# Performance work log

Hardware: AMD Instinct MI355X
Metric: run time of the kernel (lower is better)

The kernel has to match this reference:

```python
import jax, jax.numpy as jnp
import numpy as np

DIM = 2048          # SDR dimension
CTX = 512           # top-down context (grid code) dimension
B = 8192            # batch of independent samples
N_PV = DIM // 4     # 512 PV interneurons
N_SV = DIM // 8     # 256 SOM/VIP interneurons
ALPHA_POS = 1.0 / 10.0   # dt / tau_pos
ALPHA_NEG = 1.0 / 10.0   # dt / tau_neg


def setup_inputs() -> dict:
    key = jax.random.key(0)
    ks = jax.random.split(key, 14)
    sc = 1.0 / np.sqrt(DIM)
    sc_sv = 1.0 / np.sqrt(N_SV)
    xav = np.sqrt(6.0 / (CTX + DIM))  # xavier uniform bound for predictor
    u = lambda k, shp, s: jax.random.uniform(k, shp, dtype=jnp.float32) * s
    return {
        "x_batch": jax.random.uniform(ks[0], (B, DIM), dtype=jnp.float32),
        "context_batch": jax.random.normal(ks[1], (B, CTX), dtype=jnp.float32),
        "r_pos_batch": jax.random.uniform(ks[2], (B, DIM), dtype=jnp.float32),
        "r_neg_batch": jax.random.uniform(ks[3], (B, DIM), dtype=jnp.float32),
        "W_pred": jax.random.uniform(ks[4], (DIM, CTX), jnp.float32, -xav, xav),
        "b_pred": jnp.zeros((DIM,), jnp.float32),
        "W_pv1_ff": u(ks[5], (N_PV, DIM), sc),
        "W_pv2_td": u(ks[6], (N_PV, DIM), sc),
        "W_vip_td": u(ks[7], (N_SV, DIM), sc),
        "W_som_in": u(ks[8], (N_SV, DIM), sc),
        "W_vip_som": u(ks[9], (N_SV, N_SV), sc_sv),
        "W_inh_pe_pos": u(ks[10], (DIM, N_PV), sc),
        "W_inh_pe_neg": u(ks[11], (DIM, N_PV), sc),
        "W_som_dend": u(ks[12], (DIM, N_SV), sc),
    }


def reference(x_batch, context_batch, r_pos_batch, r_neg_batch,
              W_pred, b_pred, W_pv1_ff, W_pv2_td, W_vip_td, W_som_in,
              W_vip_som, W_inh_pe_pos, W_inh_pe_neg, W_som_dend):
    relu = jax.nn.relu
    # top-down prediction: (B, CTX) @ (CTX, DIM) -> (B, DIM)
    predicted = context_batch @ W_pred.T + b_pred
    # interneuron circuit (Nemati 2025)
    r_pv1 = relu(x_batch @ W_pv1_ff.T)                               # (B, N_PV)
    r_pv2 = relu(predicted @ W_pv2_td.T)                             # (B, N_PV)
    r_vip = relu(predicted @ W_vip_td.T)                             # (B, N_SV)
    r_som = relu(relu(x_batch @ W_som_in.T) - r_vip @ W_vip_som.T)   # (B, N_SV)
    # signed prediction errors with somatic/dendritic inhibition
    pe_pos = relu(x_batch - predicted - r_pv2 @ W_inh_pe_pos.T)
    pe_neg = relu(predicted - x_batch - r_pv1 @ W_inh_pe_neg.T - r_som @ W_som_dend.T)
    # low-pass temporal filter of PE states
    new_r_pos = (1.0 - ALPHA_POS) * r_pos_batch + ALPHA_POS * pe_pos
    new_r_neg = (1.0 - ALPHA_NEG) * r_neg_batch + ALPHA_NEG * pe_neg
    return (new_r_pos, new_r_neg)
```

## Files before the change

### kernel.cpp

```cpp
#include <hip/hip_runtime.h>
#include <hip/hip_bf16.h>
#include <stdint.h>
#include <stddef.h>

#define DIMV 2048
#define CTXV 512
#define BV   8192
#define NPV  512
#define NSV  256

typedef __attribute__((ext_vector_type(8))) __bf16 bf16x8;
typedef __attribute__((ext_vector_type(4))) float f32x4;

enum { EPI_BIAS = 0, EPI_RELU = 1, EPI_SUBR = 2, EPI_FILT = 3 };

__device__ __forceinline__ void gload_lds16(const void* g, void* l) {
    __builtin_amdgcn_global_load_lds(
        (const __attribute__((address_space(1))) unsigned int*)g,
        (__attribute__((address_space(3))) unsigned int*)l,
        16, 0, 0);
}

struct CvtArgs {
    const float* src[11];
    __bf16*      dst[11];
};

__global__ __launch_bounds__(256) void cvt_all(CvtArgs a) {
    constexpr int NSEG = 11;
    constexpr unsigned cum[NSEG + 1] = {
        0u, 2097152u, 2621440u, 2752512u, 2883584u, 3014656u,
        3080192u, 3145728u, 3153920u, 3284992u, 3416064u, 3481600u};
    const unsigned total = cum[NSEG];
    for (unsigned c = blockIdx.x * blockDim.x + threadIdx.x; c < total;
         c += gridDim.x * blockDim.x) {
        const float* sp = a.src[0];
        __bf16*      dp = a.dst[0];
        unsigned     base = 0;
#pragma unroll
        for (int t = 1; t < NSEG; ++t) {
            const bool g = (c >= cum[t]);
            sp   = g ? a.src[t] : sp;
            dp   = g ? a.dst[t] : dp;
            base = g ? cum[t] : base;
        }
        const unsigned off = (c - base) * 8u;
        f32x4 v0 = *(const f32x4*)(sp + off);
        f32x4 v1 = *(const f32x4*)(sp + off + 4);
        bf16x8 o;
#pragma unroll
        for (int e = 0; e < 4; ++e) { o[e] = (__bf16)v0[e]; o[e + 4] = (__bf16)v1[e]; }
        *(bf16x8*)(dp + off) = o;
    }
}

template <int EPI>
__global__ __launch_bounds__(256)
void pe_gemm(const __bf16* __restrict__ A, int ldA,
             const __bf16* __restrict__ A2, int ldA2, int ksA,
             const __bf16* __restrict__ W1, int ldW1,
             const __bf16* __restrict__ W1k2, int ldW1k2, int ksW,
             const __bf16* __restrict__ W2, int ldW2,
             int NB1, int N1cols, int N2cols, int K, int nbx,
             const float* __restrict__ bias,
             const __bf16* __restrict__ subp,
             const __bf16* __restrict__ predb, const float* __restrict__ xf,
             float sgn, const float* __restrict__ rold,
             void* __restrict__ out1, void* __restrict__ out2)
{
    __shared__ __align__(16) __bf16 ldsA[128 * 32];
    __shared__ __align__(16) __bf16 ldsB[128 * 32];
    char* ldsAb = (char*)ldsA;
    char* ldsBb = (char*)ldsB;

    const int nwg = gridDim.x;
    const int bid = blockIdx.x;
    const int wg  = (bid & 7) * (nwg >> 3) + (bid >> 3);
    const int bx  = wg % nbx;
    const int by  = wg / nbx;
    const int m0  = bx * 128;
    const int n0  = by * 128;

    const bool reg2   = (W2 != nullptr) && (n0 >= NB1);
    const __bf16* Wa  = reg2 ? W2 : W1;
    const __bf16* Wb  = W1k2;
    const int wlda    = reg2 ? ldW2 : ldW1;
    const int wldb    = ldW1k2;
    const int kswcur  = reg2 ? K : ksW;
    const int nrow0   = reg2 ? (n0 - NB1) : n0;

    const int tid  = threadIdx.x;
    const int wave = tid >> 6;
    const int lane = tid & 63;
    const int lhi  = lane >> 4;
    const int llo  = lane & 15;
    const int wr   = wave >> 1;
    const int wc   = wave & 1;

    const f32x4 fzero = {0.f, 0.f, 0.f, 0.f};
    f32x4 acc[4][4];
#pragma unroll
    for (int i = 0; i < 4; ++i)
#pragma unroll
        for (int j = 0; j < 4; ++j) acc[i][j] = fzero;

    const int rins = lane >> 2;
    const int ch   = lane & 3;

    for (int k0 = 0; k0 < K; k0 += 32) {
        __syncthreads();
#pragma unroll
        for (int half = 0; half < 2; ++half) {
            const int rt = wave * 32 + half * 16 + rins;
            const int kc = ch ^ ((rt >> 1) & 3);
            const int kg = k0 + kc * 8;
            {
                const __bf16* src = (kg < ksA)
                    ? A  + (size_t)(m0 + rt) * ldA  + kg
                    : A2 + (size_t)(m0 + rt) * ldA2 + (kg - ksA);
                gload_lds16(src, ldsAb + wave * 2048 + half * 1024);
            }
            {
                const __bf16* src = (kg < kswcur)
                    ? Wa + (size_t)(nrow0 + rt) * wlda + kg
                    : Wb + (size_t)(nrow0 + rt) * wldb + (kg - kswcur);
                gload_lds16(src, ldsBb + wave * 2048 + half * 1024);
            }
        }
        __syncthreads();

        bf16x8 af[4], bfr[4];
#pragma unroll
        for (int i = 0; i < 4; ++i) {
            const int r  = wr * 64 + i * 16 + llo;
            const int pc = lhi ^ ((r >> 1) & 3);
            af[i] = *(const bf16x8*)(ldsAb + r * 64 + pc * 16);
        }
#pragma unroll
        for (int j = 0; j < 4; ++j) {
            const int r  = wc * 64 + j * 16 + llo;
            const int pc = lhi ^ ((r >> 1) & 3);
            bfr[j] = *(const bf16x8*)(ldsBb + r * 64 + pc * 16);
        }
#pragma unroll
        for (int i = 0; i < 4; ++i)
#pragma unroll
            for (int j = 0; j < 4; ++j)
                acc[i][j] = __builtin_amdgcn_mfma_f32_16x16x32_bf16(af[i], bfr[j], acc[i][j], 0, 0, 0);
    }

#pragma unroll
    for (int i = 0; i < 4; ++i) {
#pragma unroll
        for (int j = 0; j < 4; ++j) {
            const int colg = n0 + wc * 64 + j * 16 + llo;
#pragma unroll
            for (int r = 0; r < 4; ++r) {
                const int rowg = m0 + wr * 64 + i * 16 + lhi * 4 + r;
                float v = acc[i][j][r];
                if constexpr (EPI == EPI_BIAS) {
                    v += bias[colg];
                    ((__bf16*)out1)[(size_t)rowg * N1cols + colg] = (__bf16)v;
                } else if constexpr (EPI == EPI_RELU) {
                    v = fmaxf(v, 0.f);
                    if (colg < NB1)
                        ((__bf16*)out1)[(size_t)rowg * N1cols + colg] = (__bf16)v;
                    else
                        ((__bf16*)out2)[(size_t)rowg * N2cols + (colg - NB1)] = (__bf16)v;
                } else if constexpr (EPI == EPI_SUBR) {
                    const size_t idx = (size_t)rowg * N1cols + colg;
                    v = fmaxf((float)subp[idx] - v, 0.f);
                    ((__bf16*)out1)[idx] = (__bf16)v;
                } else {
                    const size_t idx = (size_t)rowg * 2048 + colg;
                    const float d = sgn * (xf[idx] - (float)predb[idx]) - v;
                    ((float*)out1)[idx] = 0.9f * rold[idx] + 0.1f * fmaxf(d, 0.f);
                }
            }
        }
    }
}

extern "C" void kernel_launch(void* const* d_in, const int* in_sizes, int n_in,
                              void* d_out, int out_size, void* d_ws, size_t ws_size,
                              hipStream_t stream) {
    (void)in_sizes; (void)n_in; (void)out_size; (void)ws_size;

    const float* x       = (const float*)d_in[0];
    const float* ctx     = (const float*)d_in[1];
    const float* r_pos   = (const float*)d_in[2];
    const float* r_neg   = (const float*)d_in[3];
    const float* Wpred   = (const float*)d_in[4];
    const float* bpred   = (const float*)d_in[5];
    const float* Wpv1    = (const float*)d_in[6];
    const float* Wpv2    = (const float*)d_in[7];
    const float* Wvip    = (const float*)d_in[8];
    const float* Wsomin  = (const float*)d_in[9];
    const float* Wvipsom = (const float*)d_in[10];
    const float* Wpepos  = (const float*)d_in[11];
    const float* Wpeneg  = (const float*)d_in[12];
    const float* Wsomd   = (const float*)d_in[13];

    char* ws = (char*)d_ws;
    __bf16* x_bf      = (__bf16*)ws; ws += (size_t)BV * DIMV * 2;
    __bf16* ctx_bf    = (__bf16*)ws; ws += (size_t)BV * CTXV * 2;
    __bf16* pred_bf   = (__bf16*)ws; ws += (size_t)BV * DIMV * 2;
    __bf16* rpv1_bf   = (__bf16*)ws; ws += (size_t)BV * NPV * 2;
    __bf16* rpv2_bf   = (__bf16*)ws; ws += (size_t)BV * NPV * 2;
    __bf16* rvip_bf   = (__bf16*)ws; ws += (size_t)BV * NSV * 2;
    __bf16* ssom_bf   = (__bf16*)ws; ws += (size_t)BV * NSV * 2;
    __bf16* rsom_bf   = (__bf16*)ws; ws += (size_t)BV * NSV * 2;
    __bf16* Wpred_bf  = (__bf16*)ws; ws += (size_t)DIMV * CTXV * 2;
    __bf16* Wpv1_bf   = (__bf16*)ws; ws += (size_t)NPV * DIMV * 2;
    __bf16* Wpv2_bf   = (__bf16*)ws; ws += (size_t)NPV * DIMV * 2;
    __bf16* Wvip_bf   = (__bf16*)ws; ws += (size_t)NSV * DIMV * 2;
    __bf16* Wsomin_bf = (__bf16*)ws; ws += (size_t)NSV * DIMV * 2;
    __bf16* Wvipsom_bf= (__bf16*)ws; ws += (size_t)NSV * NSV * 2;
    __bf16* Wpepos_bf = (__bf16*)ws; ws += (size_t)DIMV * NPV * 2;
    __bf16* Wpeneg_bf = (__bf16*)ws; ws += (size_t)DIMV * NPV * 2;
    __bf16* Wsomd_bf  = (__bf16*)ws; ws += (size_t)DIMV * NSV * 2;

    float* out_pos = (float*)d_out;
    float* out_neg = out_pos + (size_t)BV * DIMV;

    CvtArgs ca;
    ca.src[0] = x;       ca.dst[0] = x_bf;
    ca.src[1] = ctx;     ca.dst[1] = ctx_bf;
    ca.src[2] = Wpred;   ca.dst[2] = Wpred_bf;
    ca.src[3] = Wpv1;    ca.dst[3] = Wpv1_bf;
    ca.src[4] = Wpv2;    ca.dst[4] = Wpv2_bf;
    ca.src[5] = Wvip;    ca.dst[5] = Wvip_bf;
    ca.src[6] = Wsomin;  ca.dst[6] = Wsomin_bf;
    ca.src[7] = Wvipsom; ca.dst[7] = Wvipsom_bf;
    ca.src[8] = Wpepos;  ca.dst[8] = Wpepos_bf;
    ca.src[9] = Wpeneg;  ca.dst[9] = Wpeneg_bf;
    ca.src[10] = Wsomd;  ca.dst[10] = Wsomd_bf;
    cvt_all<<<dim3(2048), dim3(256), 0, stream>>>(ca);

    dim3 blk(256);

    pe_gemm<EPI_BIAS><<<dim3(1024), blk, 0, stream>>>(
        ctx_bf, CTXV, nullptr, 0, CTXV,
        Wpred_bf, CTXV, nullptr, 0, CTXV, nullptr, 0,
        DIMV, DIMV, 0, CTXV, 64,
        bpred, nullptr, nullptr, nullptr, 0.f, nullptr, pred_bf, nullptr);

    pe_gemm<EPI_RELU><<<dim3(384), blk, 0, stream>>>(
        x_bf, DIMV, nullptr, 0, DIMV,
        Wpv1_bf, DIMV, nullptr, 0, DIMV, Wsomin_bf, DIMV,
        NPV, NPV, NSV, DIMV, 64,
        nullptr, nullptr, nullptr, nullptr, 0.f, nullptr, rpv1_bf, ssom_bf);

    pe_gemm<EPI_RELU><<<dim3(384), blk, 0, stream>>>(
        pred_bf, DIMV, nullptr, 0, DIMV,
        Wpv2_bf, DIMV, nullptr, 0, DIMV, Wvip_bf, DIMV,
        NPV, NPV, NSV, DIMV, 64,
        nullptr, nullptr, nullptr, nullptr, 0.f, nullptr, rpv2_bf, rvip_bf);

    pe_gemm<EPI_SUBR><<<dim3(128), blk, 0, stream>>>(
        rvip_bf, NSV, nullptr, 0, NSV,
        Wvipsom_bf, NSV, nullptr, 0, NSV, nullptr, 0,
        NSV, NSV, 0, NSV, 64,
        nullptr, ssom_bf, nullptr, nullptr, 0.f, nullptr, rsom_bf, nullptr);

    pe_gemm<EPI_FILT><<<dim3(1024), blk, 0, stream>>>(
        rpv2_bf, NPV, nullptr, 0, NPV,
        Wpepos_bf, NPV, nullptr, 0, NPV, nullptr, 0,
        DIMV, DIMV, 0, NPV, 64,
        nullptr, nullptr, pred_bf, x, 1.f, r_pos, out_pos, nullptr);

    pe_gemm<EPI_FILT><<<dim3(1024), blk, 0, stream>>>(
        rpv1_bf, NPV, rsom_bf, NSV, NPV,
        Wpeneg_bf, NPV, Wsomd_bf, NSV, NPV, nullptr, 0,
        DIMV, DIMV, 0, NPV + NSV, 64,
        nullptr, nullptr, pred_bf, x, -1.f, r_neg, out_neg, nullptr);
}
```

Before: 353.9 us.

## Fuse pos/neg filter GEMMs into one kernel and vectorize epilogues

Merges the two final prediction-error GEMM kernels into a single kernel that accumulates both the positive and negative paths per tile and writes both filtered outputs. The x minus prediction term is computed once per tile from bf16 copies instead of being read twice from fp32. The MFMA operand order is swapped so each lane holds four consecutive columns, which allows 4-wide vector stores and loads in all epilogues instead of scalar strided ones. The fused kernel holds twice as many accumulators, which raises register pressure and may reduce occupancy. Using bf16 x in the difference also slightly lowers precision.

```diff
diff --git a/kernel.cpp b/kernel.cpp
--- a/kernel.cpp
+++ b/kernel.cpp
@@ -10,9 +10,10 @@
 #define NSV  256
 
 typedef __attribute__((ext_vector_type(8))) __bf16 bf16x8;
+typedef __attribute__((ext_vector_type(4))) __bf16 bf16x4;
 typedef __attribute__((ext_vector_type(4))) float f32x4;
 
-enum { EPI_BIAS = 0, EPI_RELU = 1, EPI_SUBR = 2, EPI_FILT = 3 };
+enum { EPI_BIAS = 0, EPI_RELU = 1, EPI_SUBR = 2 };
 
 __device__ __forceinline__ void gload_lds16(const void* g, void* l) {
     __builtin_amdgcn_global_load_lds(
@@ -54,48 +55,70 @@
     }
 }
 
+#define GEMM_PREAMBLE(NBX)                                        \
+    __shared__ __align__(16) __bf16 ldsA[128 * 32];               \
+    __shared__ __align__(16) __bf16 ldsB[128 * 32];               \
+    char* ldsAb = (char*)ldsA;                                    \
+    char* ldsBb = (char*)ldsB;                                    \
+    const int nwg = gridDim.x;                                    \
+    const int bid = blockIdx.x;                                   \
+    const int wg  = (bid & 7) * (nwg >> 3) + (bid >> 3);          \
+    const int bx  = wg % (NBX);                                   \
+    const int by  = wg / (NBX);                                   \
+    const int m0  = bx * 128;                                     \
+    const int n0  = by * 128;                                     \
+    const int tid  = threadIdx.x;                                 \
+    const int wave = tid >> 6;                                    \
+    const int lane = tid & 63;                                    \
+    const int lhi  = lane >> 4;                                   \
+    const int llo  = lane & 15;                                   \
+    const int wr   = wave >> 1;                                   \
+    const int wc   = wave & 1;                                    \
+    const int rins = lane >> 2;                                   \
+    const int ch   = lane & 3;
+
+#define STAGE_TILE(Asrc, ldA, Wsrc, ldW, kofs)                                    \
+    _Pragma("unroll")                                                             \
+    for (int half = 0; half < 2; ++half) {                                        \
+        const int rt = wave * 32 + half * 16 + rins;                              \
+        const int kc = ch ^ ((rt >> 1) & 3);                                      \
+        const int kk = (kofs) + kc * 8;                                           \
+        gload_lds16((Asrc) + (size_t)(m0 + rt) * (ldA) + kk,                      \
+                    ldsAb + wave * 2048 + half * 1024);                           \
+        gload_lds16((Wsrc) + (size_t)(n0r + rt) * (ldW) + kk,                     \
+                    ldsBb + wave * 2048 + half * 1024);                           \
+    }
+
+#define LOAD_FRAGS(af, bfr)                                       \
+    _Pragma("unroll")                                             \
+    for (int i = 0; i < 4; ++i) {                                 \
+        const int r  = wr * 64 + i * 16 + llo;                    \
+        const int pc = lhi ^ ((r >> 1) & 3);                      \
+        af[i] = *(const bf16x8*)(ldsAb + r * 64 + pc * 16);       \
+    }                                                             \
+    _Pragma("unroll")                                             \
+    for (int j = 0; j < 4; ++j) {                                 \
+        const int r  = wc * 64 + j * 16 + llo;                    \
+        const int pc = lhi ^ ((r >> 1) & 3);                      \
+        bfr[j] = *(const bf16x8*)(ldsBb + r * 64 + pc * 16);      \
+    }
+
 template <int EPI>
 __global__ __launch_bounds__(256)
 void pe_gemm(const __bf16* __restrict__ A, int ldA,
-             const __bf16* __restrict__ A2, int ldA2, int ksA,
-             const __bf16* __restrict__ W1, int ldW1,
-             const __bf16* __restrict__ W1k2, int ldW1k2, int ksW,
-             const __bf16* __restrict__ W2, int ldW2,
-             int NB1, int N1cols, int N2cols, int K, int nbx,
+             const __bf16* __restrict__ W1, const __bf16* __restrict__ W2,
+             int ldW, int NB1, int N1cols, int N2cols, int K, int nbx,
              const float* __restrict__ bias,
              const __bf16* __restrict__ subp,
-             const __bf16* __restrict__ predb, const float* __restrict__ xf,
-             float sgn, const float* __restrict__ rold,
-             void* __restrict__ out1, void* __restrict__ out2)
+             __bf16* __restrict__ out1, __bf16* __restrict__ out2)
 {
-    __shared__ __align__(16) __bf16 ldsA[128 * 32];
-    __shared__ __align__(16) __bf16 ldsB[128 * 32];
-    char* ldsAb = (char*)ldsA;
-    char* ldsBb = (char*)ldsB;
-
-    const int nwg = gridDim.x;
-    const int bid = blockIdx.x;
-    const int wg  = (bid & 7) * (nwg >> 3) + (bid >> 3);
-    const int bx  = wg % nbx;
-    const int by  = wg / nbx;
-    const int m0  = bx * 128;
-    const int n0  = by * 128;
+    GEMM_PREAMBLE(nbx)
 
     const bool reg2   = (W2 != nullptr) && (n0 >= NB1);
     const __bf16* Wa  = reg2 ? W2 : W1;
-    const __bf16* Wb  = W1k2;
-    const int wlda    = reg2 ? ldW2 : ldW1;
-    const int wldb    = ldW1k2;
-    const int kswcur  = reg2 ? K : ksW;
-    const int nrow0   = reg2 ? (n0 - NB1) : n0;
-
-    const int tid  = threadIdx.x;
-    const int wave = tid >> 6;
-    const int lane = tid & 63;
-    const int lhi  = lane >> 4;
-    const int llo  = lane & 15;
-    const int wr   = wave >> 1;
-    const int wc   = wave & 1;
+    const int n0r     = reg2 ? (n0 - NB1) : n0;
+    __bf16* outp      = reg2 ? out2 : out1;
+    const int ldo     = reg2 ? N2cols : N1cols;
 
     const f32x4 fzero = {0.f, 0.f, 0.f, 0.f};
     f32x4 acc[4][4];
@@ -104,79 +127,113 @@
 #pragma unroll
         for (int j = 0; j < 4; ++j) acc[i][j] = fzero;
 
-    const int rins = lane >> 2;
-    const int ch   = lane & 3;
-
     for (int k0 = 0; k0 < K; k0 += 32) {
         __syncthreads();
-#pragma unroll
-        for (int half = 0; half < 2; ++half) {
-            const int rt = wave * 32 + half * 16 + rins;
-            const int kc = ch ^ ((rt >> 1) & 3);
-            const int kg = k0 + kc * 8;
-            {
-                const __bf16* src = (kg < ksA)
-                    ? A  + (size_t)(m0 + rt) * ldA  + kg
-                    : A2 + (size_t)(m0 + rt) * ldA2 + (kg - ksA);
-                gload_lds16(src, ldsAb + wave * 2048 + half * 1024);
+        STAGE_TILE(A, ldA, Wa, ldW, k0)
+        __syncthreads();
+        bf16x8 af[4], bfr[4];
+        LOAD_FRAGS(af, bfr)
+#pragma unroll
+        for (int i = 0; i < 4; ++i)
+#pragma unroll
+            for (int j = 0; j < 4; ++j)
+                acc[i][j] = __builtin_amdgcn_mfma_f32_16x16x32_bf16(bfr[j], af[i], acc[i][j], 0, 0, 0);
+    }
+
+#pragma unroll
+    for (int i = 0; i < 4; ++i) {
+#pragma unroll
+        for (int j = 0; j < 4; ++j) {
+            const int rowg = m0 + wr * 64 + i * 16 + llo;
+            const int colb = wc * 64 + j * 16 + lhi * 4;
+            const size_t idx = (size_t)rowg * ldo + (n0r + colb);
+            bf16x4 o;
+            if constexpr (EPI == EPI_BIAS) {
+                f32x4 b4 = *(const f32x4*)(bias + n0 + colb);
+#pragma unroll
+                for (int r = 0; r < 4; ++r) o[r] = (__bf16)(acc[i][j][r] + b4[r]);
+            } else if constexpr (EPI == EPI_RELU) {
+#pragma unroll
+                for (int r = 0; r < 4; ++r) o[r] = (__bf16)fmaxf(acc[i][j][r], 0.f);
+            } else {
+                bf16x4 s4 = *(const bf16x4*)(subp + idx);
+#pragma unroll
+                for (int r = 0; r < 4; ++r) o[r] = (__bf16)fmaxf((float)s4[r] - acc[i][j][r], 0.f);
             }
-            {
-                const __bf16* src = (kg < kswcur)
-                    ? Wa + (size_t)(nrow0 + rt) * wlda + kg
-                    : Wb + (size_t)(nrow0 + rt) * wldb + (kg - kswcur);
-                gload_lds16(src, ldsBb + wave * 2048 + half * 1024);
+            *(bf16x4*)(outp + idx) = o;
+        }
+    }
+}
+
+__global__ __launch_bounds__(256)
+void pe_filt_fused(const __bf16* __restrict__ Apos,
+                   const __bf16* __restrict__ Aneg1,
+                   const __bf16* __restrict__ Aneg2,
+                   const __bf16* __restrict__ Wpos,
+                   const __bf16* __restrict__ Wneg1,
+                   const __bf16* __restrict__ Wneg2,
+                   const __bf16* __restrict__ xbf,
+                   const __bf16* __restrict__ predb,
+                   const float* __restrict__ rpos, const float* __restrict__ rneg,
+                   float* __restrict__ outp, float* __restrict__ outn)
+{
+    GEMM_PREAMBLE(64)
+    const int n0r = n0;
+
+    const f32x4 fzero = {0.f, 0.f, 0.f, 0.f};
+    f32x4 accP[4][4], accN[4][4];
+#pragma unroll
+    for (int i = 0; i < 4; ++i)
+#pragma unroll
+        for (int j = 0; j < 4; ++j) { accP[i][j] = fzero; accN[i][j] = fzero; }
+
+    for (int k0 = 0; k0 < 1280; k0 += 32) {
+        __syncthreads();
+        if (k0 < 512) {
+            STAGE_TILE(Apos, 512, Wpos, 512, k0)
+        } else if (k0 < 1024) {
+            STAGE_TILE(Aneg1, 512, Wneg1, 512, k0 - 512)
+        } else {
+            STAGE_TILE(Aneg2, 256, Wneg2, 256, k0 - 1024)
+        }
+        __syncthreads();
+        bf16x8 af[4], bfr[4];
+        LOAD_FRAGS(af, bfr)
+        if (k0 < 512) {
+#pragma unroll
+            for (int i = 0; i < 4; ++i)
+#pragma unroll
+                for (int j = 0; j < 4; ++j)
+                    accP[i][j] = __builtin_amdgcn_mfma_f32_16x16x32_bf16(bfr[j], af[i], accP[i][j], 0, 0, 0);
+        } else {
+#pragma unroll
+            for (int i = 0; i < 4; ++i)
+#pragma unroll
+                for (int j = 0; j < 4; ++j)
+                    accN[i][j] = __builtin_amdgcn_mfma_f32_16x16x32_bf16(bfr[j], af[i], accN[i][j], 0, 0, 0);
+        }
+    }
+
+#pragma unroll
+    for (int i = 0; i < 4; ++i) {
+#pragma unroll
+        for (int j = 0; j < 4; ++j) {
+            const int rowg = m0 + wr * 64 + i * 16 + llo;
+            const int colg = n0 + wc * 64 + j * 16 + lhi * 4;
+            const size_t idx = (size_t)rowg * 2048 + colg;
+            f32x4 rp = *(const f32x4*)(rpos + idx);
+            f32x4 rn = *(const f32x4*)(rneg + idx);
+            bf16x4 xb = *(const bf16x4*)(xbf + idx);
+            bf16x4 pb = *(const bf16x4*)(predb + idx);
+            f32x4 op, on;
+#pragma unroll
+            for (int r = 0; r < 4; ++r) {
+                const float d = (float)xb[r] - (float)pb[r];
+                op[r] = 0.9f * rp[r] + 0.1f * fmaxf( d - accP[i][j][r], 0.f);
+                on[r] = 0.9f * rn[r] + 0.1f * fmaxf(-d - accN[i][j][r], 0.f);
             }
-        }
-        __syncthreads();
-
-        bf16x8 af[4], bfr[4];
-#pragma unroll
-        for (int i = 0; i < 4; ++i) {
-            const int r  = wr * 64 + i * 16 + llo;
-            const int pc = lhi ^ ((r >> 1) & 3);
-            af[i] = *(const bf16x8*)(ldsAb + r * 64 + pc * 16);
-        }
-#pragma unroll
-        for (int j = 0; j < 4; ++j) {
-            const int r  = wc * 64 + j * 16 + llo;
-            const int pc = lhi ^ ((r >> 1) & 3);
-            bfr[j] = *(const bf16x8*)(ldsBb + r * 64 + pc * 16);
-        }
-#pragma unroll
-        for (int i = 0; i < 4; ++i)
-#pragma unroll
-            for (int j = 0; j < 4; ++j)
-                acc[i][j] = __builtin_amdgcn_mfma_f32_16x16x32_bf16(af[i], bfr[j], acc[i][j], 0, 0, 0);
-    }
-
-#pragma unroll
-    for (int i = 0; i < 4; ++i) {
-#pragma unroll
-        for (int j = 0; j < 4; ++j) {
-            const int colg = n0 + wc * 64 + j * 16 + llo;
-#pragma unroll
-            for (int r = 0; r < 4; ++r) {
-                const int rowg = m0 + wr * 64 + i * 16 + lhi * 4 + r;
-                float v = acc[i][j][r];
-                if constexpr (EPI == EPI_BIAS) {
-                    v += bias[colg];
-                    ((__bf16*)out1)[(size_t)rowg * N1cols + colg] = (__bf16)v;
-                } else if constexpr (EPI == EPI_RELU) {
-                    v = fmaxf(v, 0.f);
-                    if (colg < NB1)
-                        ((__bf16*)out1)[(size_t)rowg * N1cols + colg] = (__bf16)v;
-                    else
-                        ((__bf16*)out2)[(size_t)rowg * N2cols + (colg - NB1)] = (__bf16)v;
-                } else if constexpr (EPI == EPI_SUBR) {
-                    const size_t idx = (size_t)rowg * N1cols + colg;
-                    v = fmaxf((float)subp[idx] - v, 0.f);
-                    ((__bf16*)out1)[idx] = (__bf16)v;
-                } else {
-                    const size_t idx = (size_t)rowg * 2048 + colg;
-                    const float d = sgn * (xf[idx] - (float)predb[idx]) - v;
-                    ((float*)out1)[idx] = 0.9f * rold[idx] + 0.1f * fmaxf(d, 0.f);
-                }
-            }
+            *(f32x4*)(outp + idx) = op;
+            *(f32x4*)(outn + idx) = on;
         }
     }
 }
@@ -240,38 +297,27 @@
     dim3 blk(256);
 
     pe_gemm<EPI_BIAS><<<dim3(1024), blk, 0, stream>>>(
-        ctx_bf, CTXV, nullptr, 0, CTXV,
-        Wpred_bf, CTXV, nullptr, 0, CTXV, nullptr, 0,
+        ctx_bf, CTXV, Wpred_bf, nullptr, CTXV,
         DIMV, DIMV, 0, CTXV, 64,
-        bpred, nullptr, nullptr, nullptr, 0.f, nullptr, pred_bf, nullptr);
+        bpred, nullptr, pred_bf, nullptr);
 
     pe_gemm<EPI_RELU><<<dim3(384), blk, 0, stream>>>(
-        x_bf, DIMV, nullptr, 0, DIMV,
-        Wpv1_bf, DIMV, nullptr, 0, DIMV, Wsomin_bf, DIMV,
+        x_bf, DIMV, Wpv1_bf, Wsomin_bf, DIMV,
         NPV, NPV, NSV, DIMV, 64,
-        nullptr, nullptr, nullptr, nullptr, 0.f, nullptr, rpv1_bf, ssom_bf);
+        nullptr, nullptr, rpv1_bf, ssom_bf);
 
     pe_gemm<EPI_RELU><<<dim3(384), blk, 0, stream>>>(
-        pred_bf, DIMV, nullptr, 0, DIMV,
-        Wpv2_bf, DIMV, nullptr, 0, DIMV, Wvip_bf, DIMV,
+        pred_bf, DIMV, Wpv2_bf, Wvip_bf, DIMV,
         NPV, NPV, NSV, DIMV, 64,
-        nullptr, nullptr, nullptr, nullptr, 0.f, nullptr, rpv2_bf, rvip_bf);
+        nullptr, nullptr, rpv2_bf, rvip_bf);
 
     pe_gemm<EPI_SUBR><<<dim3(128), blk, 0, stream>>>(
-        rvip_bf, NSV, nullptr, 0, NSV,
-        Wvipsom_bf, NSV, nullptr, 0, NSV, nullptr, 0,
+        rvip_bf, NSV, Wvipsom_bf, nullptr, NSV,
         NSV, NSV, 0, NSV, 64,
-        nullptr, ssom_bf, nullptr, nullptr, 0.f, nullptr, rsom_bf, nullptr);
-
-    pe_gemm<EPI_FILT><<<dim3(1024), blk, 0, stream>>>(
-        rpv2_bf, NPV, nullptr, 0, NPV,
-        Wpepos_bf, NPV, nullptr, 0, NPV, nullptr, 0,
-        DIMV, DIMV, 0, NPV, 64,
-        nullptr, nullptr, pred_bf, x, 1.f, r_pos, out_pos, nullptr);
-
-    pe_gemm<EPI_FILT><<<dim3(1024), blk, 0, stream>>>(
-        rpv1_bf, NPV, rsom_bf, NSV, NPV,
-        Wpeneg_bf, NPV, Wsomd_bf, NSV, NPV, nullptr, 0,
-        DIMV, DIMV, 0, NPV + NSV, 64,
-        nullptr, nullptr, pred_bf, x, -1.f, r_neg, out_neg, nullptr);
-}
+        nullptr, ssom_bf, rsom_bf, nullptr);
+
+    pe_filt_fused<<<dim3(1024), blk, 0, stream>>>(
+        rpv2_bf, rpv1_bf, rsom_bf,
+        Wpepos_bf, Wpeneg_bf, Wsomd_bf,
+        x_bf, pred_bf, r_pos, r_neg, out_pos, out_neg);
+}
```

Result: slower. 394.7 us (+11.5%).
